# Performance work log

Measured on AMD Instinct MI355X. Metric: run time of the kernel, lower is better.

Reference implementation:

```python
import jax, jax.numpy as jnp
import numpy as np

EPS = 1e-5  # torch nn.LayerNorm default eps
DIST_CUTOFF = 10.0


def _ln(x, g, b):
    m = jnp.mean(x, axis=-1, keepdims=True)
    v = jnp.mean((x - m) ** 2, axis=-1, keepdims=True)
    return (x - m) * jax.lax.rsqrt(v + EPS) * g + b


def setup_inputs() -> dict:
    key = jax.random.key(0)
    ks = iter(jax.random.split(key, 48))
    L, B, N, D, H = 4, 1, 256, 128, 512
    IN = D + N  # 384 == node_dim + edge_dim + node_dim under the consistency constraint
    r = lambda *s: jax.random.normal(next(ks), s, jnp.float32) * 0.02
    return dict(
        nodes=jax.random.normal(next(ks), (B, N, D), jnp.float32),
        coords=jax.random.normal(next(ks), (B, N, 3), jnp.float32),
        ee_w=r(1, D), ee_b=jnp.zeros(D), ee_g=jnp.ones(D), ee_bt=jnp.zeros(D),
        nu1_w=r(L, IN, H), nu1_b=jnp.zeros((L, H)), nu_g=jnp.ones((L, H)), nu_bt=jnp.zeros((L, H)),
        nu2_w=r(L, H, D), nu2_b=jnp.zeros((L, D)),
        eu1_w=r(L, IN, H), eu1_b=jnp.zeros((L, H)), eu_g=jnp.ones((L, H)), eu_bt=jnp.zeros((L, H)),
        eu2_w=r(L, H, D), eu2_b=jnp.zeros((L, D)),
        sp1_w=r(D, H), sp1_b=jnp.zeros(H), sp_g=jnp.ones(H), sp_bt=jnp.zeros(H),
        sp2_w=r(H, 3), sp2_b=jnp.zeros(3),
        no1_w=r(D, H), no1_b=jnp.zeros(H), no_g=jnp.ones(H), no_bt=jnp.zeros(H),
        no2_w=r(H, D), no2_b=jnp.zeros(D),
    )


def reference(nodes, coords, ee_w, ee_b, ee_g, ee_bt,
              nu1_w, nu1_b, nu_g, nu_bt, nu2_w, nu2_b,
              eu1_w, eu1_b, eu_g, eu_bt, eu2_w, eu2_b,
              sp1_w, sp1_b, sp_g, sp_bt, sp2_w, sp2_b,
              no1_w, no1_b, no_g, no_bt, no2_w, no2_b):
    B, N, D = nodes.shape
    # initialize_edges: pairwise distances -> edge embedding + adjacency
    diff = coords[:, :, None, :] - coords[:, None, :, :]           # [B,N,N,3]
    sq = jnp.sum(diff * diff, axis=-1)                              # [B,N,N]
    dist = jnp.where(sq > 0, jnp.sqrt(jnp.where(sq > 0, sq, 1.0)), 0.0)
    adj = (dist < DIST_CUTOFF).astype(nodes.dtype)                  # [B,N,N]
    edges = jax.nn.relu(_ln(dist[..., None] @ ee_w + ee_b, ee_g, ee_bt))  # [B,N,N,D]

    def step(carry, p):
        nd, ed = carry
        w1n, b1n, gn, btn, w2n, b2n, w1e, b1e, ge, bte, w2e, b2e = p
        # messages: einsum('bijk,bik->bij', edges*adj[...,None], nodes)
        msgs = adj * jnp.einsum('bijk,bik->bij', ed, nd)            # [B,N,N]
        ni = jnp.concatenate([nd, msgs], axis=-1)                    # [B,N,D+N]
        nd_new = nd + jax.nn.relu(_ln(ni @ w1n + b1n, gn, btn)) @ w2n + b2n
        pairs = jnp.concatenate([
            jnp.broadcast_to(nd[:, :, None, :], (B, N, N, D)),
            jnp.broadcast_to(nd[:, None, :, :], (B, N, N, D))], axis=-1)  # [B,N,N,2D]
        ei = jnp.concatenate([ed, pairs], axis=-1)                   # [B,N,N,3D]
        ed_new = ed + jax.nn.relu(_ln(ei @ w1e + b1e, ge, bte)) @ w2e + b2e
        return (nd_new, ed_new), None

    (nd, _ed), _ = jax.lax.scan(
        step, (nodes, edges),
        (nu1_w, nu1_b, nu_g, nu_bt, nu2_w, nu2_b,
         eu1_w, eu1_b, eu_g, eu_bt, eu2_w, eu2_b))

    nodes_out = jax.nn.relu(_ln(nd @ no1_w + no1_b, no_g, no_bt)) @ no2_w + no2_b
    coords_pred = jax.nn.relu(_ln(nodes_out @ sp1_w + sp1_b, sp_g, sp_bt)) @ sp2_w + sp2_b
    return nodes_out, coords_pred
```

## Files before the change

### kernel.cpp

```cpp
#include <hip/hip_runtime.h>

#define LNEPS 1e-5f

typedef unsigned short ushort_t;
typedef __attribute__((ext_vector_type(8))) short short8;
typedef __attribute__((ext_vector_type(4))) float f32x4;

__device__ inline unsigned short f2b(float f) {
    union { float f; unsigned int u; } c; c.f = f;
    unsigned int u = c.u;
    unsigned int r = (u + 0x7FFFu + ((u >> 16) & 1u)) >> 16;
    return (unsigned short)r;
}

__global__ void k_convw(const float* __restrict__ w1, const float* __restrict__ w2,
                        ushort_t* __restrict__ w1P, ushort_t* __restrict__ w2P) {
    int idx = blockIdx.x * 256 + threadIdx.x;
    if (idx < 65536) {
        int l = idx >> 14, r = idx & 16383;
        int c = r >> 9;  r &= 511;
        int kb = r >> 6, lane = r & 63;
        int col = c * 16 + (lane & 15);
        int k0 = kb * 32 + (lane >> 4) * 8;
        ushort_t o[8];
        #pragma unroll
        for (int e = 0; e < 8; ++e) {
            int kl = k0 + e;
            int row = kl < 128 ? kl : kl + 128;
            o[e] = f2b(w1[((size_t)l * 384 + row) * 512 + col]);
        }
        *(uint4*)(w1P + (size_t)idx * 8) = *(uint4*)o;
    }
    if (idx < 32768) {
        int l = idx >> 13, r = idx & 8191;
        int c2 = r >> 10; r &= 1023;
        int kbg = r >> 6, lane = r & 63;
        int col = c2 * 16 + (lane & 15);
        int k0 = kbg * 32 + (lane >> 4) * 8;
        ushort_t o[8];
        #pragma unroll
        for (int e = 0; e < 8; ++e)
            o[e] = f2b(w2[((size_t)l * 512 + k0 + e) * 128 + col]);
        *(uint4*)(w2P + (size_t)idx * 8) = *(uint4*)o;
    }
}

__global__ void k_init(const float* __restrict__ coords, const float* __restrict__ nodes,
                       const float* __restrict__ ee_w, const float* __restrict__ ee_b,
                       const float* __restrict__ ee_g, const float* __restrict__ ee_bt,
                       float* __restrict__ ed, ushort_t* __restrict__ edb,
                       float* __restrict__ adjf, float* __restrict__ msgs) {
    int r = blockIdx.x * 4 + (threadIdx.x >> 6);
    int lane = threadIdx.x & 63;
    int i = r >> 8, j = r & 255;
    float dx = coords[i * 3 + 0] - coords[j * 3 + 0];
    float dy = coords[i * 3 + 1] - coords[j * 3 + 1];
    float dz = coords[i * 3 + 2] - coords[j * 3 + 2];
    float sq = dx * dx + dy * dy + dz * dz;
    float dist = sq > 0.f ? sqrtf(sq) : 0.f;
    float adjv = dist < 10.f ? 1.f : 0.f;
    if (lane == 0) adjf[r] = adjv;
    float e0 = dist * ee_w[lane] + ee_b[lane];
    float e1 = dist * ee_w[lane + 64] + ee_b[lane + 64];
    float s = e0 + e1, q = e0 * e0 + e1 * e1;
    #pragma unroll
    for (int off = 1; off < 64; off <<= 1) {
        s += __shfl_xor(s, off, 64);
        q += __shfl_xor(q, off, 64);
    }
    float mean = s * (1.f / 128.f);
    float var = q * (1.f / 128.f) - mean * mean;
    float rs = rsqrtf(var + LNEPS);
    float e0r = fmaxf((e0 - mean) * rs * ee_g[lane] + ee_bt[lane], 0.f);
    float e1r = fmaxf((e1 - mean) * rs * ee_g[lane + 64] + ee_bt[lane + 64], 0.f);
    ed[(size_t)r * 128 + lane]       = e0r;
    ed[(size_t)r * 128 + lane + 64]  = e1r;
    edb[(size_t)r * 128 + lane]      = f2b(e0r);
    edb[(size_t)r * 128 + lane + 64] = f2b(e1r);
    float d = e0r * nodes[(i << 7) + lane] + e1r * nodes[(i << 7) + 64 + lane];
    #pragma unroll
    for (int off = 1; off < 64; off <<= 1) d += __shfl_xor(d, off, 64);
    if (lane == 0) msgs[r] = adjv * d;
}

__global__ __launch_bounds__(512) void k_pre(
    const float* __restrict__ nd, const float* __restrict__ W1,
    const float* __restrict__ b1,
    float* __restrict__ cI, ushort_t* __restrict__ ndb) {
    __shared__ float ndl[128];
    int p = blockIdx.x, t = threadIdx.x;
    if (t < 128) {
        float v = nd[(size_t)p * 128 + t];
        ndl[t] = v;
        ndb[(size_t)p * 128 + t] = f2b(v);
    }
    __syncthreads();
    const float* wm = W1 + (size_t)128 * 512 + t;
    float a1 = b1[t];
    #pragma unroll 4
    for (int k = 0; k < 128; ++k) a1 += ndl[k] * wm[(size_t)k * 512];
    cI[(size_t)p * 512 + t] = a1;
}

__global__ __launch_bounds__(512) void k_mlp(
    const float* __restrict__ in0, int w0, const float* __restrict__ in1, int w1n,
    const float* __restrict__ W1, const float* __restrict__ b1,
    const float* __restrict__ g, const float* __restrict__ bt,
    const float* __restrict__ W2, const float* __restrict__ b2, int O,
    const float* __restrict__ res, float* __restrict__ out) {
    __shared__ float ni[384];
    __shared__ float hsh[512];
    __shared__ float part[4][128];
    __shared__ float red[16];
    int row = blockIdx.x;
    int t = threadIdx.x;
    int K = w0 + w1n;
    if (t < w0) ni[t] = in0[(size_t)row * w0 + t];
    else if (t < K) ni[t] = in1[(size_t)row * w1n + (t - w0)];
    __syncthreads();
    float acc = b1[t];
    #pragma unroll 4
    for (int k = 0; k < K; ++k) acc += ni[k] * W1[(size_t)k * 512 + t];
    float s = acc, q = acc * acc;
    #pragma unroll
    for (int off = 1; off < 64; off <<= 1) {
        s += __shfl_xor(s, off, 64);
        q += __shfl_xor(q, off, 64);
    }
    int wv = t >> 6;
    if ((t & 63) == 0) { red[wv] = s; red[8 + wv] = q; }
    __syncthreads();
    float S = 0.f, Q = 0.f;
    #pragma unroll
    for (int w = 0; w < 8; ++w) { S += red[w]; Q += red[8 + w]; }
    float mean = S * (1.f / 512.f);
    float var = Q * (1.f / 512.f) - mean * mean;
    float rs = rsqrtf(var + LNEPS);
    hsh[t] = fmaxf((acc - mean) * rs * g[t] + bt[t], 0.f);
    __syncthreads();
    int qd = t >> 7, c = t & 127;
    float pacc = 0.f;
    if (c < O) {
        #pragma unroll 4
        for (int kk = 0; kk < 128; ++kk)
            pacc += hsh[qd * 128 + kk] * W2[(size_t)(qd * 128 + kk) * O + c];
    }
    part[qd][c] = pacc;
    __syncthreads();
    if (t < O) {
        float v = part[0][t] + part[1][t] + part[2][t] + part[3][t] + b2[t];
        if (res) v += res[(size_t)row * O + t];
        out[(size_t)row * O + t] = v;
    }
}

__global__ __launch_bounds__(512, 4) void k_edge(
    float* ed, ushort_t* edb, const ushort_t* __restrict__ ndb,
    const float* __restrict__ cIg, const ushort_t* __restrict__ w1P,
    const float* __restrict__ g, const float* __restrict__ bt,
    const ushort_t* __restrict__ w2P, const float* __restrict__ b2,
    const float* __restrict__ ndn, const float* __restrict__ adjf,
    float* __restrict__ msgs) {
    __shared__ char smem[70144];
    const int tid = threadIdx.x;
    const int w = tid >> 6, lane = tid & 63;
    const int l15 = lane & 15, lhi = lane >> 4;
    const int rbase = blockIdx.x * 64;
    const int ib = rbase >> 8;
    const int jbase = rbase & 255;

    #pragma unroll
    for (int it = 0; it < 4; ++it) {
        int c = tid + it * 512;
        int row = c >> 5, q = c & 31;
        uint4 pk;
        if (q < 16) pk = *(const uint4*)(edb + (size_t)(rbase + row) * 128 + q * 8);
        else        pk = *(const uint4*)(ndb + (size_t)(jbase + row) * 128 + (q - 16) * 8);
        *(uint4*)(smem + row * 512 + ((q ^ (row & 7)) * 16)) = pk;
    }
    __syncthreads();

    f32x4 acc[4][4];
    f32x4 zero = {0.f, 0.f, 0.f, 0.f};
    #pragma unroll
    for (int m = 0; m < 4; ++m)
        #pragma unroll
        for (int n = 0; n < 4; ++n) acc[m][n] = zero;

    const int cw = w * 64;
    #pragma unroll 2
    for (int kb = 0; kb < 8; ++kb) {
        short8 a[4];
        #pragma unroll
        for (int m = 0; m < 4; ++m) {
            int row = m * 16 + l15;
            a[m] = *(const short8*)(smem + row * 512 + (((kb * 4 + lhi) ^ (row & 7)) * 16));
        }
        #pragma unroll
        for (int n = 0; n < 4; ++n) {
            short8 b = *(const short8*)(w1P + ((((w * 4 + n) * 8 + kb) << 6) + lane) * 8);
            #pragma unroll
            for (int m = 0; m < 4; ++m)
                acc[m][n] = __builtin_amdgcn_mfma_f32_16x16x32_bf16(b, a[m], acc[m][n], 0, 0, 0);
        }
    }

    float* red = (float*)(smem + 65536);
    float* stats = (float*)(smem + 69632);
    {
        float4 ci[4];
        #pragma unroll
        for (int n = 0; n < 4; ++n)
            ci[n] = *(const float4*)(cIg + (size_t)ib * 512 + cw + n * 16 + lhi * 4);
        #pragma unroll
        for (int m = 0; m < 4; ++m) {
            float s = 0.f, q = 0.f;
            #pragma unroll
            for (int n = 0; n < 4; ++n) {
                float v0 = acc[m][n][0] + ci[n].x;
                float v1 = acc[m][n][1] + ci[n].y;
                float v2 = acc[m][n][2] + ci[n].z;
                float v3 = acc[m][n][3] + ci[n].w;
                acc[m][n][0] = v0; acc[m][n][1] = v1;
                acc[m][n][2] = v2; acc[m][n][3] = v3;
                s += v0 + v1 + v2 + v3;
                q += v0 * v0 + v1 * v1 + v2 * v2 + v3 * v3;
            }
            s += __shfl_xor(s, 16, 64);
            s += __shfl_xor(s, 32, 64);
            q += __shfl_xor(q, 16, 64);
            q += __shfl_xor(q, 32, 64);
            if (lhi == 0) {
                red[(w * 64 + m * 16 + l15) * 2 + 0] = s;
                red[(w * 64 + m * 16 + l15) * 2 + 1] = q;
            }
        }
    }
    __syncthreads();
    if (tid < 64) {
        float S = 0.f, Q = 0.f;
        #pragma unroll
        for (int ww = 0; ww < 8; ++ww) {
            S += red[(ww * 64 + tid) * 2 + 0];
            Q += red[(ww * 64 + tid) * 2 + 1];
        }
        float mean = S * (1.f / 512.f);
        float var = Q * (1.f / 512.f) - mean * mean;
        stats[tid * 2 + 0] = mean;
        stats[tid * 2 + 1] = rsqrtf(var + LNEPS);
    }
    __syncthreads();

    {
        float4 gg[4], bb[4];
        #pragma unroll
        for (int n = 0; n < 4; ++n) {
            gg[n] = *(const float4*)(g + cw + n * 16 + lhi * 4);
            bb[n] = *(const float4*)(bt + cw + n * 16 + lhi * 4);
        }
        #pragma unroll
        for (int m = 0; m < 4; ++m) {
            int row = m * 16 + l15;
            float mean = stats[row * 2 + 0];
            float rs = stats[row * 2 + 1];
            #pragma unroll
            for (int n = 0; n < 4; ++n) {
                float v0 = fmaxf((acc[m][n][0] - mean) * rs * gg[n].x + bb[n].x, 0.f);
                float v1 = fmaxf((acc[m][n][1] - mean) * rs * gg[n].y + bb[n].y, 0.f);
                float v2 = fmaxf((acc[m][n][2] - mean) * rs * gg[n].z + bb[n].z, 0.f);
                float v3 = fmaxf((acc[m][n][3] - mean) * rs * gg[n].w + bb[n].w, 0.f);
                int p0 = cw + n * 16 + lhi * 4;
                int addr = row * 1024 + ((((p0 >> 3) ^ (row & 7))) * 16) + (p0 & 7) * 2;
                uint2 pk;
                pk.x = (unsigned)f2b(v0) | ((unsigned)f2b(v1) << 16);
                pk.y = (unsigned)f2b(v2) | ((unsigned)f2b(v3) << 16);
                *(uint2*)(smem + addr) = pk;
            }
        }
    }
    __syncthreads();

    const int rt = w >> 1, ch2 = w & 1;
    f32x4 acc2[4];
    #pragma unroll
    for (int n2 = 0; n2 < 4; ++n2) acc2[n2] = zero;
    const int arow = rt * 16 + l15;
    #pragma unroll 2
    for (int kbg = 0; kbg < 16; ++kbg) {
        short8 a = *(const short8*)(smem + arow * 1024 + (((kbg * 4 + lhi) ^ (arow & 7)) * 16));
        #pragma unroll
        for (int n2 = 0; n2 < 4; ++n2) {
            short8 b = *(const short8*)(w2P + ((((ch2 * 4 + n2) * 16 + kbg) << 6) + lane) * 8);
            acc2[n2] = __builtin_amdgcn_mfma_f32_16x16x32_bf16(b, a, acc2[n2], 0, 0, 0);
        }
    }

    float partial = 0.f;
    {
        const int row = rt * 16 + l15;
        #pragma unroll
        for (int n2 = 0; n2 < 4; ++n2) {
            int col0 = ch2 * 64 + n2 * 16 + lhi * 4;
            size_t goff = (size_t)(rbase + row) * 128 + col0;
            float4 r4 = *(const float4*)(ed + goff);
            float4 b4 = *(const float4*)(b2 + col0);
            float4 n4 = *(const float4*)(ndn + (size_t)ib * 128 + col0);
            float o0 = acc2[n2][0] + b4.x + r4.x;
            float o1 = acc2[n2][1] + b4.y + r4.y;
            float o2 = acc2[n2][2] + b4.z + r4.z;
            float o3 = acc2[n2][3] + b4.w + r4.w;
            float4 o4 = {o0, o1, o2, o3};
            *(float4*)(ed + goff) = o4;
            uint2 pk;
            pk.x = (unsigned)f2b(o0) | ((unsigned)f2b(o1) << 16);
            pk.y = (unsigned)f2b(o2) | ((unsigned)f2b(o3) << 16);
            *(uint2*)(edb + goff) = pk;
            partial += o0 * n4.x + o1 * n4.y + o2 * n4.z + o3 * n4.w;
        }
    }
    partial += __shfl_xor(partial, 16, 64);
    partial += __shfl_xor(partial, 32, 64);
    float* msum = (float*)(smem + 65536);
    if (lhi == 0) msum[ch2 * 64 + rt * 16 + l15] = partial;
    __syncthreads();
    if (tid < 64) msgs[rbase + tid] = adjf[rbase + tid] * (msum[tid] + msum[64 + tid]);
}

extern "C" void kernel_launch(void* const* d_in, const int* in_sizes, int n_in,
                              void* d_out, int out_size, void* d_ws, size_t ws_size,
                              hipStream_t stream) {
    const float* nodes  = (const float*)d_in[0];
    const float* coords = (const float*)d_in[1];
    const float* ee_w   = (const float*)d_in[2];
    const float* ee_b   = (const float*)d_in[3];
    const float* ee_g   = (const float*)d_in[4];
    const float* ee_bt  = (const float*)d_in[5];
    const float* nu1_w  = (const float*)d_in[6];
    const float* nu1_b  = (const float*)d_in[7];
    const float* nu_g   = (const float*)d_in[8];
    const float* nu_bt  = (const float*)d_in[9];
    const float* nu2_w  = (const float*)d_in[10];
    const float* nu2_b  = (const float*)d_in[11];
    const float* eu1_w  = (const float*)d_in[12];
    const float* eu1_b  = (const float*)d_in[13];
    const float* eu_g   = (const float*)d_in[14];
    const float* eu_bt  = (const float*)d_in[15];
    const float* eu2_w  = (const float*)d_in[16];
    const float* eu2_b  = (const float*)d_in[17];
    const float* sp1_w  = (const float*)d_in[18];
    const float* sp1_b  = (const float*)d_in[19];
    const float* sp_g   = (const float*)d_in[20];
    const float* sp_bt  = (const float*)d_in[21];
    const float* sp2_w  = (const float*)d_in[22];
    const float* sp2_b  = (const float*)d_in[23];
    const float* no1_w  = (const float*)d_in[24];
    const float* no1_b  = (const float*)d_in[25];
    const float* no_g   = (const float*)d_in[26];
    const float* no_bt  = (const float*)d_in[27];
    const float* no2_w  = (const float*)d_in[28];
    const float* no2_b  = (const float*)d_in[29];

    char* p = (char*)d_ws;
    float* ed      = (float*)p;     p += (size_t)65536 * 128 * 4;
    ushort_t* edb  = (ushort_t*)p;  p += (size_t)65536 * 128 * 2;
    float* ndA     = (float*)p;     p += 256 * 128 * 4;
    float* ndB     = (float*)p;     p += 256 * 128 * 4;
    ushort_t* ndb  = (ushort_t*)p;  p += 256 * 128 * 2;
    float* msgs    = (float*)p;     p += 65536 * 4;
    float* adjf    = (float*)p;     p += 65536 * 4;
    float* cI      = (float*)p;     p += 256 * 512 * 4;
    ushort_t* w1P  = (ushort_t*)p;  p += (size_t)4 * 131072 * 2;
    ushort_t* w2P  = (ushort_t*)p;  p += (size_t)4 * 65536 * 2;

    k_convw<<<256, 256, 0, stream>>>(eu1_w, eu2_w, w1P, w2P);
    k_init<<<16384, 256, 0, stream>>>(coords, nodes, ee_w, ee_b, ee_g, ee_bt,
                                      ed, edb, adjf, msgs);

    const float* nd_cur = nodes;
    float* nd_bufs[2] = {ndA, ndB};
    for (int l = 0; l < 4; ++l) {
        float* nd_next = nd_bufs[l & 1];
        k_pre<<<256, 512, 0, stream>>>(nd_cur, eu1_w + (size_t)l * 384 * 512,
                                       eu1_b + l * 512, cI, ndb);
        k_mlp<<<256, 512, 0, stream>>>(nd_cur, 128, msgs, 256,
            nu1_w + (size_t)l * 384 * 512, nu1_b + l * 512, nu_g + l * 512, nu_bt + l * 512,
            nu2_w + (size_t)l * 512 * 128, nu2_b + l * 128, 128, nd_cur, nd_next);
        k_edge<<<1024, 512, 0, stream>>>(ed, edb, ndb, cI,
            w1P + (size_t)l * 131072, eu_g + l * 512, eu_bt + l * 512,
            w2P + (size_t)l * 65536, eu2_b + l * 128,
            nd_next, adjf, msgs);
        nd_cur = nd_next;
    }

    float* out_nodes  = (float*)d_out;
    float* out_coords = out_nodes + 32768;
    k_mlp<<<256, 512, 0, stream>>>(nd_cur, 128, nullptr, 0,
        no1_w, no1_b, no_g, no_bt, no2_w, no2_b, 128, nullptr, out_nodes);
    k_mlp<<<256, 512, 0, stream>>>(out_nodes, 128, nullptr, 0,
        sp1_w, sp1_b, sp_g, sp_bt, sp2_w, sp2_b, 3, nullptr, out_coords);
}
```

Before: 639.7 us.

## Halve edge-kernel LDS by staging hidden activations in two K-halves

The 64x512 bf16 hidden activation tile is now written to shared memory in two 256-column halves, each consumed by the second GEMM before the next half is staged. This roughly halves the LDS footprint and raises the launch-bounds occupancy hint from 4 to 8 blocks per CU. In exchange, the activations must stay in registers until their half is written, and two extra barriers are added, which may increase register pressure and serialize the second GEMM.

```diff
diff --git a/kernel.cpp b/kernel.cpp
--- a/kernel.cpp
+++ b/kernel.cpp
@@ -154,14 +154,14 @@
     }
 }
 
-__global__ __launch_bounds__(512, 4) void k_edge(
+__global__ __launch_bounds__(512, 8) void k_edge(
     float* ed, ushort_t* edb, const ushort_t* __restrict__ ndb,
     const float* __restrict__ cIg, const ushort_t* __restrict__ w1P,
     const float* __restrict__ g, const float* __restrict__ bt,
     const ushort_t* __restrict__ w2P, const float* __restrict__ b2,
     const float* __restrict__ ndn, const float* __restrict__ adjf,
     float* __restrict__ msgs) {
-    __shared__ char smem[70144];
+    __shared__ char smem[37376];
     const int tid = threadIdx.x;
     const int w = tid >> 6, lane = tid & 63;
     const int l15 = lane & 15, lhi = lane >> 4;
@@ -205,8 +205,8 @@
         }
     }
 
-    float* red = (float*)(smem + 65536);
-    float* stats = (float*)(smem + 69632);
+    float* red = (float*)(smem + 32768);
+    float* stats = (float*)(smem + 36864);
     {
         float4 ci[4];
         #pragma unroll
@@ -265,34 +265,49 @@
             float rs = stats[row * 2 + 1];
             #pragma unroll
             for (int n = 0; n < 4; ++n) {
-                float v0 = fmaxf((acc[m][n][0] - mean) * rs * gg[n].x + bb[n].x, 0.f);
-                float v1 = fmaxf((acc[m][n][1] - mean) * rs * gg[n].y + bb[n].y, 0.f);
-                float v2 = fmaxf((acc[m][n][2] - mean) * rs * gg[n].z + bb[n].z, 0.f);
-                float v3 = fmaxf((acc[m][n][3] - mean) * rs * gg[n].w + bb[n].w, 0.f);
-                int p0 = cw + n * 16 + lhi * 4;
-                int addr = row * 1024 + ((((p0 >> 3) ^ (row & 7))) * 16) + (p0 & 7) * 2;
-                uint2 pk;
-                pk.x = (unsigned)f2b(v0) | ((unsigned)f2b(v1) << 16);
-                pk.y = (unsigned)f2b(v2) | ((unsigned)f2b(v3) << 16);
-                *(uint2*)(smem + addr) = pk;
+                acc[m][n][0] = fmaxf((acc[m][n][0] - mean) * rs * gg[n].x + bb[n].x, 0.f);
+                acc[m][n][1] = fmaxf((acc[m][n][1] - mean) * rs * gg[n].y + bb[n].y, 0.f);
+                acc[m][n][2] = fmaxf((acc[m][n][2] - mean) * rs * gg[n].z + bb[n].z, 0.f);
+                acc[m][n][3] = fmaxf((acc[m][n][3] - mean) * rs * gg[n].w + bb[n].w, 0.f);
             }
         }
     }
-    __syncthreads();
 
     const int rt = w >> 1, ch2 = w & 1;
+    const int arow = rt * 16 + l15;
     f32x4 acc2[4];
     #pragma unroll
     for (int n2 = 0; n2 < 4; ++n2) acc2[n2] = zero;
-    const int arow = rt * 16 + l15;
-    #pragma unroll 2
-    for (int kbg = 0; kbg < 16; ++kbg) {
-        short8 a = *(const short8*)(smem + arow * 1024 + (((kbg * 4 + lhi) ^ (arow & 7)) * 16));
-        #pragma unroll
-        for (int n2 = 0; n2 < 4; ++n2) {
-            short8 b = *(const short8*)(w2P + ((((ch2 * 4 + n2) * 16 + kbg) << 6) + lane) * 8);
-            acc2[n2] = __builtin_amdgcn_mfma_f32_16x16x32_bf16(b, a, acc2[n2], 0, 0, 0);
-        }
+
+    #pragma unroll
+    for (int hf = 0; hf < 2; ++hf) {
+        if ((w >> 2) == hf) {
+            const int base = (w & 3) * 64;
+            #pragma unroll
+            for (int m = 0; m < 4; ++m) {
+                int row = m * 16 + l15;
+                #pragma unroll
+                for (int n = 0; n < 4; ++n) {
+                    int p0 = base + n * 16 + lhi * 4;
+                    int addr = row * 512 + ((((p0 >> 3) ^ (row & 7))) * 16) + (p0 & 7) * 2;
+                    uint2 pk;
+                    pk.x = (unsigned)f2b(acc[m][n][0]) | ((unsigned)f2b(acc[m][n][1]) << 16);
+                    pk.y = (unsigned)f2b(acc[m][n][2]) | ((unsigned)f2b(acc[m][n][3]) << 16);
+                    *(uint2*)(smem + addr) = pk;
+                }
+            }
+        }
+        __syncthreads();
+        #pragma unroll 2
+        for (int kbg = 0; kbg < 8; ++kbg) {
+            short8 a = *(const short8*)(smem + arow * 512 + (((kbg * 4 + lhi) ^ (arow & 7)) * 16));
+            #pragma unroll
+            for (int n2 = 0; n2 < 4; ++n2) {
+                short8 b = *(const short8*)(w2P + ((((ch2 * 4 + n2) * 16 + hf * 8 + kbg) << 6) + lane) * 8);
+                acc2[n2] = __builtin_amdgcn_mfma_f32_16x16x32_bf16(b, a, acc2[n2], 0, 0, 0);
+            }
+        }
+        __syncthreads();
     }
 
     float partial = 0.f;
@@ -320,7 +335,7 @@
     }
     partial += __shfl_xor(partial, 16, 64);
     partial += __shfl_xor(partial, 32, 64);
-    float* msum = (float*)(smem + 65536);
+    float* msum = (float*)(smem + 32768);
     if (lhi == 0) msum[ch2 * 64 + rt * 16 + l15] = partial;
     __syncthreads();
     if (tid < 64) msgs[rbase + tid] = adjf[rbase + tid] * (msum[tid] + msum[64 + tid]);
```

New measurement: 2.322 ms. +262.9%, slower.
